# Kernel tuning notes

Hardware: AMD Instinct MI355X
Metric: run time of the kernel (lower is better)

The kernel has to match this reference:

```python
import math
import jax, jax.numpy as jnp
import numpy as np

H, PQ, PV = 12, 8, 12
C_S = 384
INF, EPS = 1e5, 1e-8
SOFTPLUS_INV_1 = 0.541324854612918


def _rand_rot(key, shape):
    """Random rotation matrices via normalized quaternions, shape + (3,3)."""
    q = jax.random.normal(key, shape + (4,))
    q = q / jnp.linalg.norm(q, axis=-1, keepdims=True)
    w, x, y, z = q[..., 0], q[..., 1], q[..., 2], q[..., 3]
    R = jnp.stack([
        1 - 2 * (y * y + z * z), 2 * (x * y - w * z), 2 * (x * z + w * y),
        2 * (x * y + w * z), 1 - 2 * (x * x + z * z), 2 * (y * z - w * x),
        2 * (x * z - w * y), 2 * (y * z + w * x), 1 - 2 * (x * x + y * y),
    ], axis=-1).reshape(shape + (3, 3))
    return R


def setup_inputs() -> dict:
    key = jax.random.key(0)
    ks = jax.random.split(key, 12)
    B, N1, N2 = 2, 2048, 512
    s1 = jax.random.normal(ks[0], (B, N1, C_S), dtype=jnp.float32)
    s2 = jax.random.normal(ks[1], (B, N2, C_S), dtype=jnp.float32)
    r1_rot = _rand_rot(ks[2], (B, N1)).astype(jnp.float32)
    r2_rot = _rand_rot(ks[3], (B, N2)).astype(jnp.float32)
    r1_trans = jax.random.normal(ks[4], (B, N1, 3), dtype=jnp.float32)
    r2_trans = jax.random.normal(ks[5], (B, N2, 3), dtype=jnp.float32)
    mask1 = jnp.ones((B, N1), dtype=jnp.float32)
    mask2 = jnp.ones((B, N2), dtype=jnp.float32)
    Wq = jax.random.normal(ks[6], (C_S, H * PQ * 3), dtype=jnp.float32) / math.sqrt(C_S)
    Wkv = jax.random.normal(ks[7], (C_S, H * (PQ + PV) * 3), dtype=jnp.float32) / math.sqrt(C_S)
    head_weights = jnp.full((H,), SOFTPLUS_INV_1, dtype=jnp.float32)
    Wout = jax.random.normal(ks[8], (H * PV * 4, C_S), dtype=jnp.float32) * 0.02
    bout = jnp.zeros((C_S,), dtype=jnp.float32)
    return {"s1": s1, "s2": s2, "r1_rot": r1_rot, "r1_trans": r1_trans,
            "r2_rot": r2_rot, "r2_trans": r2_trans, "mask1": mask1, "mask2": mask2,
            "Wq": Wq, "Wkv": Wkv, "head_weights": head_weights,
            "Wout": Wout, "bout": bout}


def reference(s1, s2, r1_rot, r1_trans, r2_rot, r2_trans, mask1, mask2,
              Wq, Wkv, head_weights, Wout, bout):
    B, N1, _ = s1.shape
    N2 = s2.shape[1]

    # query points: linear -> [B,N1,3,H,PQ] (torch split/stack layout) -> local [B,N1,H,PQ,3]
    q = jnp.moveaxis((s1 @ Wq).reshape(B, N1, 3, H, PQ), 2, -1)
    # rigid apply: R x + t (global frame)
    q = jnp.einsum('bimn,bihpn->bihpm', r1_rot, q) + r1_trans[:, :, None, None, :]

    kv = jnp.moveaxis((s2 @ Wkv).reshape(B, N2, 3, H, PQ + PV), 2, -1)
    kv = jnp.einsum('bjmn,bjhpn->bjhpm', r2_rot, kv) + r2_trans[:, :, None, None, :]
    k, v = kv[..., :PQ, :], kv[..., PQ:, :]  # [B,N2,H,PQ,3], [B,N2,H,PV,3]

    # sum_p ||q_p - k_p||^2 via norm expansion (avoids [B,N1,N2,H,PQ,3] tensor)
    qn = jnp.sum(q * q, axis=(-1, -2))                     # [B,N1,H]
    kn = jnp.sum(k * k, axis=(-1, -2))                     # [B,N2,H]
    cross = jnp.einsum('bihpc,bjhpc->bijh', q, k)          # [B,N1,N2,H]
    d2 = qn[:, :, None, :] + kn[:, None, :, :] - 2.0 * cross

    hw = jax.nn.softplus(head_weights) * math.sqrt(1.0 / (3 * (PQ * 9.0 / 2)))
    att = jnp.transpose(-0.5 * d2 * hw, (0, 3, 1, 2))      # [B,H,N1,N2]
    bias = INF * (mask1[:, :, None] * mask2[:, None, :] - 1.0)
    a = jax.nn.softmax(att + bias[:, None], axis=-1)

    o = jnp.einsum('bhij,bjhpc->bihpc', a, v)              # [B,N1,H,PV,3]
    # rigid invert_apply: R^T (x - t), back into local frame of residue i
    o_loc = jnp.einsum('bimn,bihpm->bihpn', r1_rot, o - r1_trans[:, :, None, None, :])

    dists = jnp.sqrt(jnp.sum(o_loc * o_loc, axis=-1) + EPS)   # [B,N1,H,PV]
    o_flat = o_loc.reshape(B, N1, H * PV, 3)
    feats = jnp.concatenate([o_flat[..., 0], o_flat[..., 1], o_flat[..., 2],
                             dists.reshape(B, N1, H * PV)], axis=-1)
    return feats @ Wout + bout
```

## Files before the change

### kernel.cpp

```cpp
#include <hip/hip_runtime.h>
#include <math.h>

#define B_ 2
#define N1_ 2048
#define N2_ 512
#define CS_ 384
#define H_ 12
#define PQ_ 8
#define PV_ 12
#define PKV_ 20
#define CQ_ (H_*PQ_*3)
#define CKV_ (H_*PKV_*3)
#define INF_ 100000.0f
#define HW_SCALE_ 0.09622504486493764f

typedef __attribute__((ext_vector_type(8))) short bf16x8;
typedef __attribute__((ext_vector_type(4))) float f32x4;

__device__ inline unsigned short f2bf(float x) {
  unsigned u = __float_as_uint(x);
  u += 0x7fffu + ((u >> 16) & 1u);
  return (unsigned short)(u >> 16);
}

#define PREP_S1_  1536
#define PREP_S2_  384
#define PREP_WQ_  432
#define PREP_WKV_ 1080
#define PREP_WO_  864
#define PREP_QPAD_ 192
#define PREP_VPAD_ 72
#define PREP_KN_  12
__global__ __launch_bounds__(256) void prep_kernel(
    const float* __restrict__ s1, const float* __restrict__ s2,
    const float* __restrict__ Wq, const float* __restrict__ Wkv,
    const float* __restrict__ Wout,
    unsigned short* __restrict__ s1b, unsigned short* __restrict__ s2b,
    unsigned short* __restrict__ wqT, unsigned short* __restrict__ wkvT,
    unsigned short* __restrict__ woutT, unsigned short* __restrict__ qgb,
    unsigned short* __restrict__ vtb, float* __restrict__ kn)
{
  int blk = blockIdx.x, t = threadIdx.x;
  if (blk < PREP_S1_) {
    int idx = (blk*256 + t) * 4;
    float4 v = *(const float4*)(s1 + idx);
    ushort4 o;
    o.x = f2bf(v.x); o.y = f2bf(v.y); o.z = f2bf(v.z); o.w = f2bf(v.w);
    *(ushort4*)(s1b + idx) = o;
  } else if (blk < PREP_S1_ + PREP_S2_) {
    int idx = ((blk - PREP_S1_)*256 + t) * 4;
    float4 v = *(const float4*)(s2 + idx);
    ushort4 o;
    o.x = f2bf(v.x); o.y = f2bf(v.y); o.z = f2bf(v.z); o.w = f2bf(v.w);
    *(ushort4*)(s2b + idx) = o;
  } else if (blk < PREP_S1_ + PREP_S2_ + PREP_WQ_) {
    int o = (blk - PREP_S1_ - PREP_S2_)*256 + t;
    int n = o / CS_, k = o % CS_;
    wqT[o] = f2bf(Wq[(size_t)k*CQ_ + n]);
  } else if (blk < PREP_S1_ + PREP_S2_ + PREP_WQ_ + PREP_WKV_) {
    int o = (blk - PREP_S1_ - PREP_S2_ - PREP_WQ_)*256 + t;
    int n = o / CS_, k = o % CS_;
    wkvT[o] = f2bf(Wkv[(size_t)k*CKV_ + n]);
  } else if (blk < PREP_S1_ + PREP_S2_ + PREP_WQ_ + PREP_WKV_ + PREP_WO_) {
    int o = (blk - PREP_S1_ - PREP_S2_ - PREP_WQ_ - PREP_WKV_)*256 + t;
    int n = o / 576, k = o % 576;
    woutT[o] = f2bf(Wout[(size_t)k*CS_ + n]);
  } else if (blk < PREP_S1_ + PREP_S2_ + PREP_WQ_ + PREP_WKV_ + PREP_WO_ + PREP_QPAD_) {
    int row = (blk - PREP_S1_ - PREP_S2_ - PREP_WQ_ - PREP_WKV_ - PREP_WO_)*256 + t;
    uint4 z = {0u,0u,0u,0u};
    *(uint4*)(qgb + (size_t)row*32 + 24) = z;
  } else if (blk < PREP_S1_ + PREP_S2_ + PREP_WQ_ + PREP_WKV_ + PREP_WO_ + PREP_QPAD_ + PREP_VPAD_) {
    int idx = (blk - PREP_S1_ - PREP_S2_ - PREP_WQ_ - PREP_WKV_ - PREP_WO_ - PREP_QPAD_)*256 + t;
    int f = idx * 8;
    int run = f >> 9, off = f & 511;
    int bh = run / 12, cc = 36 + run % 12;
    uint4 z = {0u,0u,0u,0u};
    *(uint4*)(vtb + ((size_t)bh*48 + cc)*512 + off) = z;
  } else {
    int idx = (blk - PREP_S1_ - PREP_S2_ - PREP_WQ_ - PREP_WKV_ - PREP_WO_ - PREP_QPAD_ - PREP_VPAD_)*256 + t;
    float4 z = {0.f,0.f,0.f,0.f};
    *(float4*)(kn + (size_t)idx*4) = z;
  }
}

__global__ __launch_bounds__(256) void qproj_mfma(
    const unsigned short* __restrict__ s1b, const unsigned short* __restrict__ wqT,
    const float* __restrict__ rot, const float* __restrict__ trans,
    unsigned short* __restrict__ qgb, float* __restrict__ qn)
{
  int wave = threadIdx.x >> 6, lane = threadIdx.x & 63;
  int col = lane & 15, g = lane >> 4;
  int wg = blockIdx.x*4 + wave;
  int strip = wg / 6;
  int nt = wg % 6;
  int i0 = strip * 16;

  f32x4 ax = {0.f,0.f,0.f,0.f}, ay = ax, az = ax;
  const unsigned short* arow = s1b + (size_t)(i0 + col)*CS_;
  const unsigned short* bx = wqT + (size_t)((nt     )*16 + col)*CS_;
  const unsigned short* by = wqT + (size_t)((nt +  6)*16 + col)*CS_;
  const unsigned short* bz = wqT + (size_t)((nt + 12)*16 + col)*CS_;
  #pragma unroll
  for (int k = 0; k < CS_; k += 32) {
    bf16x8 a = *(const bf16x8*)(arow + k + g*8);
    ax = __builtin_amdgcn_mfma_f32_16x16x32_bf16(a, *(const bf16x8*)(bx + k + g*8), ax, 0,0,0);
    ay = __builtin_amdgcn_mfma_f32_16x16x32_bf16(a, *(const bf16x8*)(by + k + g*8), ay, 0,0,0);
    az = __builtin_amdgcn_mfma_f32_16x16x32_bf16(a, *(const bf16x8*)(bz + k + g*8), az, 0,0,0);
  }

  int p = nt*16 + col;
  int h = p >> 3, pq = p & 7;
  float qsum[4];
  #pragma unroll
  for (int r = 0; r < 4; ++r) {
    int row = i0 + g*4 + r;
    const float* R  = rot   + (size_t)row*9;
    const float* tr = trans + (size_t)row*3;
    float x = ax[r], y = ay[r], z = az[r];
    float g0 = R[0]*x + R[1]*y + R[2]*z + tr[0];
    float g1 = R[3]*x + R[4]*y + R[5]*z + tr[1];
    float g2 = R[6]*x + R[7]*y + R[8]*z + tr[2];
    int b = row >> 11, i = row & (N1_-1);
    size_t base = ((size_t)(b*H_ + h)*N1_ + i)*32 + pq*3;
    qgb[base]   = f2bf(g0);
    qgb[base+1] = f2bf(g1);
    qgb[base+2] = f2bf(g2);
    qsum[r] = g0*g0 + g1*g1 + g2*g2;
  }
  #pragma unroll
  for (int r = 0; r < 4; ++r) {
    qsum[r] += __shfl_xor(qsum[r], 1);
    qsum[r] += __shfl_xor(qsum[r], 2);
    qsum[r] += __shfl_xor(qsum[r], 4);
  }
  if ((col & 7) == 0) {
    int hh = nt*2 + (col >> 3);
    #pragma unroll
    for (int r = 0; r < 4; ++r) {
      int row = i0 + g*4 + r;
      int b = row >> 11, i = row & (N1_-1);
      qn[(size_t)(b*H_ + hh)*N1_ + i] = qsum[r];
    }
  }
}

__global__ __launch_bounds__(256) void kvproj_mfma(
    const unsigned short* __restrict__ s2b, const unsigned short* __restrict__ wkvT,
    const float* __restrict__ rot, const float* __restrict__ trans,
    unsigned short* __restrict__ kgb, unsigned short* __restrict__ vtb,
    float* __restrict__ kn)
{
  int wave = threadIdx.x >> 6, lane = threadIdx.x & 63;
  int col = lane & 15, g = lane >> 4;
  int wg = blockIdx.x*4 + wave;
  int strip = wg / 15;
  int nt = wg % 15;
  int row0 = strip * 16;

  f32x4 ax = {0.f,0.f,0.f,0.f}, ay = ax, az = ax;
  const unsigned short* arow = s2b + (size_t)(row0 + col)*CS_;
  const unsigned short* bx = wkvT + (size_t)(nt*16       + col)*CS_;
  const unsigned short* by = wkvT + (size_t)(nt*16 + 240 + col)*CS_;
  const unsigned short* bz = wkvT + (size_t)(nt*16 + 480 + col)*CS_;
  #pragma unroll
  for (int k = 0; k < CS_; k += 32) {
    bf16x8 a = *(const bf16x8*)(arow + k + g*8);
    ax = __builtin_amdgcn_mfma_f32_16x16x32_bf16(a, *(const bf16x8*)(bx + k + g*8), ax, 0,0,0);
    ay = __builtin_amdgcn_mfma_f32_16x16x32_bf16(a, *(const bf16x8*)(by + k + g*8), ay, 0,0,0);
    az = __builtin_amdgcn_mfma_f32_16x16x32_bf16(a, *(const bf16x8*)(bz + k + g*8), az, 0,0,0);
  }

  int p = nt*16 + col;
  int h = p / PKV_, pp = p % PKV_;
  #pragma unroll
  for (int r = 0; r < 4; ++r) {
    int row = row0 + g*4 + r;
    const float* R  = rot   + (size_t)row*9;
    const float* tr = trans + (size_t)row*3;
    float x = ax[r], y = ay[r], z = az[r];
    float g0 = R[0]*x + R[1]*y + R[2]*z + tr[0];
    float g1 = R[3]*x + R[4]*y + R[5]*z + tr[1];
    float g2 = R[6]*x + R[7]*y + R[8]*z + tr[2];
    int b = row >> 9, j = row & (N2_-1);
    int bh = b*H_ + h;
    if (pp < PQ_) {
      size_t base = ((size_t)bh*N2_ + j)*32 + pp*3;
      kgb[base]   = f2bf(g0);
      kgb[base+1] = f2bf(g1);
      kgb[base+2] = f2bf(g2);
      if (pp == 0) {
        uint4 z4 = {0u,0u,0u,0u};
        *(uint4*)(kgb + ((size_t)bh*N2_ + j)*32 + 24) = z4;
      }
      atomicAdd(&kn[(size_t)bh*N2_ + j], g0*g0 + g1*g1 + g2*g2);
    } else {
      int comp = (pp - PQ_)*3;
      size_t base = ((size_t)bh*48 + comp)*512 + j;
      vtb[base]        = f2bf(g0);
      vtb[base + 512]  = f2bf(g1);
      vtb[base + 1024] = f2bf(g2);
    }
  }
}

#define RSTRIDE 72
#define OSTRIDE 52
__global__ __launch_bounds__(256) void attn_kernel(
    const unsigned short* __restrict__ qgb, const float* __restrict__ qn,
    const unsigned short* __restrict__ kgb, const unsigned short* __restrict__ vtb,
    const float* __restrict__ kn, const float* __restrict__ mask1,
    const float* __restrict__ mask2, const float* __restrict__ hwts,
    const float* __restrict__ rot, const float* __restrict__ trans,
    unsigned short* __restrict__ featsb)
{
  __shared__ __align__(16) unsigned short pstrip[4][16][RSTRIDE];
  __shared__ float o_s[4][16][OSTRIDE];
  __shared__ float l_s[4][16];

  int wave = threadIdx.x >> 6;
  int lane = threadIdx.x & 63;
  int col = lane & 15, g = lane >> 4;
  int mt = blockIdx.x*4 + wave;
  int bh = mt >> 7;
  int it = mt & 127;
  int b = bh / H_, h = bh - b*H_;

  float hw = logf(1.0f + __expf(hwts[h])) * HW_SCALE_;

  bf16x8 qa = *(const bf16x8*)(qgb + (((size_t)bh*N1_ + it*16 + col)*32 + g*8));

  float ar[4], m1r[4];
  #pragma unroll
  for (int r = 0; r < 4; ++r) {
    int ig = it*16 + g*4 + r;
    ar[r]  = fmaf(-0.5f*hw, qn[(size_t)bh*N1_ + ig], -INF_);
    m1r[r] = mask1[b*N1_ + ig] * INF_;
  }

  f32x4 ot[3];
  #pragma unroll
  for (int m = 0; m < 3; ++m) ot[m] = (f32x4){0.f,0.f,0.f,0.f};
  float l[4] = {0.f,0.f,0.f,0.f};

  const unsigned short* kbase = kgb + (size_t)bh*N2_*32;
  const unsigned short* vbase = vtb + (size_t)bh*48*512;
  const float* knp = kn + (size_t)bh*N2_;
  const float* m2p = mask2 + b*N2_;

  for (int jt = 0; jt < 8; ++jt) {
    int j0 = jt*64;
    #pragma unroll
    for (int nt = 0; nt < 4; ++nt) {
      int jg = j0 + nt*16 + col;
      bf16x8 kb = *(const bf16x8*)(kbase + ((size_t)jg*32 + g*8));
      f32x4 dotv = __builtin_amdgcn_mfma_f32_16x16x32_bf16(
          qa, kb, (f32x4){0.f,0.f,0.f,0.f}, 0, 0, 0);
      float bc  = -0.5f*hw*knp[jg];
      float m2c = m2p[jg];
      #pragma unroll
      for (int r = 0; r < 4; ++r) {
        float logit = fmaf(hw, dotv[r], fmaf(m1r[r], m2c, ar[r] + bc));
        float w = __expf(logit);
        l[r] += w;
        pstrip[wave][g*4 + r][nt*16 + col] = f2bf(w);
      }
    }
    #pragma unroll
    for (int ks = 0; ks < 2; ++ks) {
      bf16x8 pb = *(const bf16x8*)&pstrip[wave][col][ks*32 + g*8];
      #pragma unroll
      for (int mtv = 0; mtv < 3; ++mtv) {
        bf16x8 va = *(const bf16x8*)(vbase +
            ((size_t)(mtv*16 + col))*512 + j0 + ks*32 + g*8);
        ot[mtv] = __builtin_amdgcn_mfma_f32_16x16x32_bf16(va, pb, ot[mtv], 0, 0, 0);
      }
    }
  }

  #pragma unroll
  for (int r = 0; r < 4; ++r) {
    l[r] += __shfl_xor(l[r], 1);
    l[r] += __shfl_xor(l[r], 2);
    l[r] += __shfl_xor(l[r], 4);
    l[r] += __shfl_xor(l[r], 8);
  }
  if (col == 0) {
    #pragma unroll
    for (int r = 0; r < 4; ++r) l_s[wave][g*4 + r] = l[r];
  }
  #pragma unroll
  for (int mtv = 0; mtv < 3; ++mtv)
    #pragma unroll
    for (int r = 0; r < 4; ++r)
      o_s[wave][col][mtv*16 + g*4 + r] = ot[mtv][r];
  __syncthreads();

  float inv = 1.0f / l_s[wave][col];
  int ig = it*16 + col;
  int row = b*N1_ + ig;
  const float* R  = rot   + (size_t)row*9;
  const float* tr = trans + (size_t)row*3;
  float R00=R[0],R01=R[1],R02=R[2],R10=R[3],R11=R[4],R12=R[5],R20=R[6],R21=R[7],R22=R[8];
  float t0=tr[0], t1=tr[1], t2=tr[2];
  unsigned short* fb = featsb + (size_t)row*576 + h*PV_;
  #pragma unroll
  for (int p = 0; p < 3; ++p) {
    int pt = g*3 + p;
    float ox = o_s[wave][col][pt*3+0]*inv - t0;
    float oy = o_s[wave][col][pt*3+1]*inv - t1;
    float oz = o_s[wave][col][pt*3+2]*inv - t2;
    float lx = R00*ox + R10*oy + R20*oz;
    float ly = R01*ox + R11*oy + R21*oz;
    float lz = R02*ox + R12*oy + R22*oz;
    float dist = sqrtf(lx*lx + ly*ly + lz*lz + 1e-8f);
    fb[pt]       = f2bf(lx);
    fb[144 + pt] = f2bf(ly);
    fb[288 + pt] = f2bf(lz);
    fb[432 + pt] = f2bf(dist);
  }
}

__global__ __launch_bounds__(512) void outproj_mfma(
    const unsigned short* __restrict__ featsb, const unsigned short* __restrict__ woutT,
    const float* __restrict__ bout, float* __restrict__ out)
{
  int wave = threadIdx.x >> 6, lane = threadIdx.x & 63;
  int col = lane & 15, g = lane >> 4;
  int i0 = blockIdx.x * 16;
  int n0 = wave * 48;

  f32x4 acc[3];
  #pragma unroll
  for (int m = 0; m < 3; ++m) acc[m] = (f32x4){0.f,0.f,0.f,0.f};
  const unsigned short* arow = featsb + (size_t)(i0 + col)*576;
  const unsigned short* b0 = woutT + (size_t)(n0      + col)*576;
  const unsigned short* b1 = woutT + (size_t)(n0 + 16 + col)*576;
  const unsigned short* b2 = woutT + (size_t)(n0 + 32 + col)*576;
  #pragma unroll 3
  for (int k = 0; k < 576; k += 32) {
    bf16x8 a = *(const bf16x8*)(arow + k + g*8);
    acc[0] = __builtin_amdgcn_mfma_f32_16x16x32_bf16(a, *(const bf16x8*)(b0 + k + g*8), acc[0], 0,0,0);
    acc[1] = __builtin_amdgcn_mfma_f32_16x16x32_bf16(a, *(const bf16x8*)(b1 + k + g*8), acc[1], 0,0,0);
    acc[2] = __builtin_amdgcn_mfma_f32_16x16x32_bf16(a, *(const bf16x8*)(b2 + k + g*8), acc[2], 0,0,0);
  }
  #pragma unroll
  for (int t3 = 0; t3 < 3; ++t3) {
    int n = n0 + t3*16 + col;
    float bb = bout[n];
    #pragma unroll
    for (int r = 0; r < 4; ++r) {
      int row = i0 + g*4 + r;
      out[(size_t)row*CS_ + n] = acc[t3][r] + bb;
    }
  }
}

extern "C" void kernel_launch(void* const* d_in, const int* in_sizes, int n_in,
                              void* d_out, int out_size, void* d_ws, size_t ws_size,
                              hipStream_t stream) {
  const float* s1       = (const float*)d_in[0];
  const float* s2       = (const float*)d_in[1];
  const float* r1_rot   = (const float*)d_in[2];
  const float* r1_trans = (const float*)d_in[3];
  const float* r2_rot   = (const float*)d_in[4];
  const float* r2_trans = (const float*)d_in[5];
  const float* mask1    = (const float*)d_in[6];
  const float* mask2    = (const float*)d_in[7];
  const float* Wq       = (const float*)d_in[8];
  const float* Wkv      = (const float*)d_in[9];
  const float* hwts     = (const float*)d_in[10];
  const float* Wout     = (const float*)d_in[11];
  const float* bout     = (const float*)d_in[12];
  float* out = (float*)d_out;

  float* qn = (float*)d_ws;
  float* kn = qn + (size_t)B_*H_*N1_;
  unsigned short* featsb = (unsigned short*)(kn + (size_t)B_*H_*N2_);
  unsigned short* qgb  = featsb + (size_t)B_*N1_*576;
  unsigned short* kgb  = qgb  + (size_t)B_*H_*N1_*32;
  unsigned short* vtb  = kgb  + (size_t)B_*H_*N2_*32;
  unsigned short* s1b  = vtb  + (size_t)B_*H_*48*512;
  unsigned short* s2b  = s1b  + (size_t)B_*N1_*CS_;
  unsigned short* wqT  = s2b  + (size_t)B_*N2_*CS_;
  unsigned short* wkvT = wqT  + (size_t)CQ_*CS_;
  unsigned short* woutT= wkvT + (size_t)CKV_*CS_;

  int prep_blocks = PREP_S1_+PREP_S2_+PREP_WQ_+PREP_WKV_+PREP_WO_+PREP_QPAD_+PREP_VPAD_+PREP_KN_;
  prep_kernel<<<prep_blocks, 256, 0, stream>>>(
      s1, s2, Wq, Wkv, Wout, s1b, s2b, wqT, wkvT, woutT, qgb, vtb, kn);
  qproj_mfma<<<384, 256, 0, stream>>>(s1b, wqT, r1_rot, r1_trans, qgb, qn);
  kvproj_mfma<<<240, 256, 0, stream>>>(s2b, wkvT, r2_rot, r2_trans, kgb, vtb, kn);
  attn_kernel<<<(B_*H_*(N1_/16))/4, 256, 0, stream>>>(qgb, qn, kgb, vtb, kn, mask1, mask2,
                                                      hwts, r1_rot, r1_trans, featsb);
  outproj_mfma<<<256, 512, 0, stream>>>(featsb, woutT, bout, out);
}
```

Baseline: 163.5 us.

## Fuse activation bf16 conversion into projections and tile weight transposes via LDS

Drops the separate fp32-to-bf16 conversion passes for s1/s2 and converts activations on the fly inside the q/kv projection MFMA loops. Weight transposes in the prep kernel now use a 32x32 LDS tile so both reads and writes are coalesced, replacing the strided per-element gather. The q padding zeroing moves into the qproj epilogue. This cuts prep traffic and blocks, but the projections now read fp32 activations (twice the bytes), and each tile's rows are converted redundantly by every wave that shares them.

```diff
diff --git a/kernel.cpp b/kernel.cpp
--- a/kernel.cpp
+++ b/kernel.cpp
@@ -23,68 +23,76 @@
   return (unsigned short)(u >> 16);
 }
 
-#define PREP_S1_  1536
-#define PREP_S2_  384
-#define PREP_WQ_  432
-#define PREP_WKV_ 1080
-#define PREP_WO_  864
-#define PREP_QPAD_ 192
-#define PREP_VPAD_ 72
-#define PREP_KN_  12
+__device__ inline bf16x8 cvt8(const float* __restrict__ p) {
+  float4 a = *(const float4*)p;
+  float4 b = *(const float4*)(p + 4);
+  bf16x8 r;
+  r[0] = (short)f2bf(a.x); r[1] = (short)f2bf(a.y);
+  r[2] = (short)f2bf(a.z); r[3] = (short)f2bf(a.w);
+  r[4] = (short)f2bf(b.x); r[5] = (short)f2bf(b.y);
+  r[6] = (short)f2bf(b.z); r[7] = (short)f2bf(b.w);
+  return r;
+}
+
+#define TQ_   108
+#define TKV_  276
+#define TWO_  216
+#define VPAD_ 72
+#define KN_   12
 __global__ __launch_bounds__(256) void prep_kernel(
-    const float* __restrict__ s1, const float* __restrict__ s2,
     const float* __restrict__ Wq, const float* __restrict__ Wkv,
     const float* __restrict__ Wout,
-    unsigned short* __restrict__ s1b, unsigned short* __restrict__ s2b,
     unsigned short* __restrict__ wqT, unsigned short* __restrict__ wkvT,
-    unsigned short* __restrict__ woutT, unsigned short* __restrict__ qgb,
+    unsigned short* __restrict__ woutT,
     unsigned short* __restrict__ vtb, float* __restrict__ kn)
 {
+  __shared__ float lds[32][33];
   int blk = blockIdx.x, t = threadIdx.x;
-  if (blk < PREP_S1_) {
-    int idx = (blk*256 + t) * 4;
-    float4 v = *(const float4*)(s1 + idx);
-    ushort4 o;
-    o.x = f2bf(v.x); o.y = f2bf(v.y); o.z = f2bf(v.z); o.w = f2bf(v.w);
-    *(ushort4*)(s1b + idx) = o;
-  } else if (blk < PREP_S1_ + PREP_S2_) {
-    int idx = ((blk - PREP_S1_)*256 + t) * 4;
-    float4 v = *(const float4*)(s2 + idx);
-    ushort4 o;
-    o.x = f2bf(v.x); o.y = f2bf(v.y); o.z = f2bf(v.z); o.w = f2bf(v.w);
-    *(ushort4*)(s2b + idx) = o;
-  } else if (blk < PREP_S1_ + PREP_S2_ + PREP_WQ_) {
-    int o = (blk - PREP_S1_ - PREP_S2_)*256 + t;
-    int n = o / CS_, k = o % CS_;
-    wqT[o] = f2bf(Wq[(size_t)k*CQ_ + n]);
-  } else if (blk < PREP_S1_ + PREP_S2_ + PREP_WQ_ + PREP_WKV_) {
-    int o = (blk - PREP_S1_ - PREP_S2_ - PREP_WQ_)*256 + t;
-    int n = o / CS_, k = o % CS_;
-    wkvT[o] = f2bf(Wkv[(size_t)k*CKV_ + n]);
-  } else if (blk < PREP_S1_ + PREP_S2_ + PREP_WQ_ + PREP_WKV_ + PREP_WO_) {
-    int o = (blk - PREP_S1_ - PREP_S2_ - PREP_WQ_ - PREP_WKV_)*256 + t;
-    int n = o / 576, k = o % 576;
-    woutT[o] = f2bf(Wout[(size_t)k*CS_ + n]);
-  } else if (blk < PREP_S1_ + PREP_S2_ + PREP_WQ_ + PREP_WKV_ + PREP_WO_ + PREP_QPAD_) {
-    int row = (blk - PREP_S1_ - PREP_S2_ - PREP_WQ_ - PREP_WKV_ - PREP_WO_)*256 + t;
-    uint4 z = {0u,0u,0u,0u};
-    *(uint4*)(qgb + (size_t)row*32 + 24) = z;
-  } else if (blk < PREP_S1_ + PREP_S2_ + PREP_WQ_ + PREP_WKV_ + PREP_WO_ + PREP_QPAD_ + PREP_VPAD_) {
-    int idx = (blk - PREP_S1_ - PREP_S2_ - PREP_WQ_ - PREP_WKV_ - PREP_WO_ - PREP_QPAD_)*256 + t;
+  int rr0 = t >> 5, cc = t & 31;
+
+  const float* src = nullptr; unsigned short* dst = nullptr;
+  int K = 0, N = 0, k0 = 0, n0 = 0;
+  if (blk < TQ_) {
+    src = Wq; dst = wqT; K = 384; N = CQ_;
+    k0 = (blk % 12) * 32; n0 = (blk / 12) * 32;
+  } else if (blk < TQ_ + TKV_) {
+    int b2 = blk - TQ_;
+    src = Wkv; dst = wkvT; K = 384; N = CKV_;
+    k0 = (b2 % 12) * 32; n0 = (b2 / 12) * 32;
+  } else if (blk < TQ_ + TKV_ + TWO_) {
+    int b3 = blk - TQ_ - TKV_;
+    src = Wout; dst = woutT; K = 576; N = CS_;
+    k0 = (b3 % 18) * 32; n0 = (b3 / 18) * 32;
+  } else if (blk < TQ_ + TKV_ + TWO_ + VPAD_) {
+    int idx = (blk - TQ_ - TKV_ - TWO_)*256 + t;
     int f = idx * 8;
     int run = f >> 9, off = f & 511;
-    int bh = run / 12, cc = 36 + run % 12;
+    int bh = run / 12, cc2 = 36 + run % 12;
     uint4 z = {0u,0u,0u,0u};
-    *(uint4*)(vtb + ((size_t)bh*48 + cc)*512 + off) = z;
+    *(uint4*)(vtb + ((size_t)bh*48 + cc2)*512 + off) = z;
+    return;
   } else {
-    int idx = (blk - PREP_S1_ - PREP_S2_ - PREP_WQ_ - PREP_WKV_ - PREP_WO_ - PREP_QPAD_ - PREP_VPAD_)*256 + t;
+    int idx = (blk - TQ_ - TKV_ - TWO_ - VPAD_)*256 + t;
     float4 z = {0.f,0.f,0.f,0.f};
     *(float4*)(kn + (size_t)idx*4) = z;
+    return;
+  }
+
+  #pragma unroll
+  for (int rr = 0; rr < 4; ++rr) {
+    int r = rr0 + rr*8;
+    if (n0 + cc < N) lds[r][cc] = src[(size_t)(k0 + r)*N + n0 + cc];
+  }
+  __syncthreads();
+  #pragma unroll
+  for (int rr = 0; rr < 4; ++rr) {
+    int r = rr0 + rr*8;
+    if (n0 + r < N) dst[(size_t)(n0 + r)*K + k0 + cc] = f2bf(lds[cc][r]);
   }
 }
 
 __global__ __launch_bounds__(256) void qproj_mfma(
-    const unsigned short* __restrict__ s1b, const unsigned short* __restrict__ wqT,
+    const float* __restrict__ s1, const unsigned short* __restrict__ wqT,
     const float* __restrict__ rot, const float* __restrict__ trans,
     unsigned short* __restrict__ qgb, float* __restrict__ qn)
 {
@@ -96,13 +104,13 @@
   int i0 = strip * 16;
 
   f32x4 ax = {0.f,0.f,0.f,0.f}, ay = ax, az = ax;
-  const unsigned short* arow = s1b + (size_t)(i0 + col)*CS_;
+  const float* arow = s1 + (size_t)(i0 + col)*CS_;
   const unsigned short* bx = wqT + (size_t)((nt     )*16 + col)*CS_;
   const unsigned short* by = wqT + (size_t)((nt +  6)*16 + col)*CS_;
   const unsigned short* bz = wqT + (size_t)((nt + 12)*16 + col)*CS_;
   #pragma unroll
   for (int k = 0; k < CS_; k += 32) {
-    bf16x8 a = *(const bf16x8*)(arow + k + g*8);
+    bf16x8 a = cvt8(arow + k + g*8);
     ax = __builtin_amdgcn_mfma_f32_16x16x32_bf16(a, *(const bf16x8*)(bx + k + g*8), ax, 0,0,0);
     ay = __builtin_amdgcn_mfma_f32_16x16x32_bf16(a, *(const bf16x8*)(by + k + g*8), ay, 0,0,0);
     az = __builtin_amdgcn_mfma_f32_16x16x32_bf16(a, *(const bf16x8*)(bz + k + g*8), az, 0,0,0);
@@ -121,10 +129,14 @@
     float g1 = R[3]*x + R[4]*y + R[5]*z + tr[1];
     float g2 = R[6]*x + R[7]*y + R[8]*z + tr[2];
     int b = row >> 11, i = row & (N1_-1);
-    size_t base = ((size_t)(b*H_ + h)*N1_ + i)*32 + pq*3;
-    qgb[base]   = f2bf(g0);
-    qgb[base+1] = f2bf(g1);
-    qgb[base+2] = f2bf(g2);
+    size_t rbase = ((size_t)(b*H_ + h)*N1_ + i)*32;
+    qgb[rbase + pq*3]     = f2bf(g0);
+    qgb[rbase + pq*3 + 1] = f2bf(g1);
+    qgb[rbase + pq*3 + 2] = f2bf(g2);
+    if (pq == 7) {
+      uint4 z4 = {0u,0u,0u,0u};
+      *(uint4*)(qgb + rbase + 24) = z4;
+    }
     qsum[r] = g0*g0 + g1*g1 + g2*g2;
   }
   #pragma unroll
@@ -145,7 +157,7 @@
 }
 
 __global__ __launch_bounds__(256) void kvproj_mfma(
-    const unsigned short* __restrict__ s2b, const unsigned short* __restrict__ wkvT,
+    const float* __restrict__ s2, const unsigned short* __restrict__ wkvT,
     const float* __restrict__ rot, const float* __restrict__ trans,
     unsigned short* __restrict__ kgb, unsigned short* __restrict__ vtb,
     float* __restrict__ kn)
@@ -158,13 +170,13 @@
   int row0 = strip * 16;
 
   f32x4 ax = {0.f,0.f,0.f,0.f}, ay = ax, az = ax;
-  const unsigned short* arow = s2b + (size_t)(row0 + col)*CS_;
+  const float* arow = s2 + (size_t)(row0 + col)*CS_;
   const unsigned short* bx = wkvT + (size_t)(nt*16       + col)*CS_;
   const unsigned short* by = wkvT + (size_t)(nt*16 + 240 + col)*CS_;
   const unsigned short* bz = wkvT + (size_t)(nt*16 + 480 + col)*CS_;
   #pragma unroll
   for (int k = 0; k < CS_; k += 32) {
-    bf16x8 a = *(const bf16x8*)(arow + k + g*8);
+    bf16x8 a = cvt8(arow + k + g*8);
     ax = __builtin_amdgcn_mfma_f32_16x16x32_bf16(a, *(const bf16x8*)(bx + k + g*8), ax, 0,0,0);
     ay = __builtin_amdgcn_mfma_f32_16x16x32_bf16(a, *(const bf16x8*)(by + k + g*8), ay, 0,0,0);
     az = __builtin_amdgcn_mfma_f32_16x16x32_bf16(a, *(const bf16x8*)(bz + k + g*8), az, 0,0,0);
@@ -379,17 +391,14 @@
   unsigned short* qgb  = featsb + (size_t)B_*N1_*576;
   unsigned short* kgb  = qgb  + (size_t)B_*H_*N1_*32;
   unsigned short* vtb  = kgb  + (size_t)B_*H_*N2_*32;
-  unsigned short* s1b  = vtb  + (size_t)B_*H_*48*512;
-  unsigned short* s2b  = s1b  + (size_t)B_*N1_*CS_;
-  unsigned short* wqT  = s2b  + (size_t)B_*N2_*CS_;
+  unsigned short* wqT  = vtb  + (size_t)B_*H_*48*512;
   unsigned short* wkvT = wqT  + (size_t)CQ_*CS_;
   unsigned short* woutT= wkvT + (size_t)CKV_*CS_;
 
-  int prep_blocks = PREP_S1_+PREP_S2_+PREP_WQ_+PREP_WKV_+PREP_WO_+PREP_QPAD_+PREP_VPAD_+PREP_KN_;
-  prep_kernel<<<prep_blocks, 256, 0, stream>>>(
-      s1, s2, Wq, Wkv, Wout, s1b, s2b, wqT, wkvT, woutT, qgb, vtb, kn);
-  qproj_mfma<<<384, 256, 0, stream>>>(s1b, wqT, r1_rot, r1_trans, qgb, qn);
-  kvproj_mfma<<<240, 256, 0, stream>>>(s2b, wkvT, r2_rot, r2_trans, kgb, vtb, kn);
+  prep_kernel<<<TQ_+TKV_+TWO_+VPAD_+KN_, 256, 0, stream>>>(
+      Wq, Wkv, Wout, wqT, wkvT, woutT, vtb, kn);
+  qproj_mfma<<<384, 256, 0, stream>>>(s1, wqT, r1_rot, r1_trans, qgb, qn);
+  kvproj_mfma<<<240, 256, 0, stream>>>(s2, wkvT, r2_rot, r2_trans, kgb, vtb, kn);
   attn_kernel<<<(B_*H_*(N1_/16))/4, 256, 0, stream>>>(qgb, qn, kgb, vtb, kn, mask1, mask2,
                                                       hwts, r1_rot, r1_trans, featsb);
   outproj_mfma<<<256, 512, 0, stream>>>(featsb, woutT, bout, out);
```

Measured after the change: 162.6 us. No clear change (-0.5%).
